# Kernel tuning notes

Hardware: AMD Instinct MI355X
Metric: run time of the kernel (lower is better)

The kernel has to match this reference:

```python
import jax, jax.numpy as jnp
import numpy as np

ITERATIONS = 20  # Resonator(iterations=20)
B, F, V, D = 128, 4, 2048, 4096


def _hardsign(x):
    # bipolar normalization used by MAP-VSA multiset(normalize=True); ties -> +1
    return jnp.where(x >= 0, 1.0, -1.0).astype(x.dtype)


def setup_inputs() -> dict:
    key = jax.random.key(0)
    k1, k2 = jax.random.split(key, 2)
    # bipolar codebooks: (F, V, D)
    codebooks = _hardsign(jax.random.normal(k1, (F, V, D), dtype=jnp.float32))
    # a realistic composite input: bind (elementwise product) of one codevector per factor
    idx = jax.random.randint(k2, (B, F), 0, V)                       # (B, F)
    chosen = codebooks[jnp.arange(F)[None, :], idx]                  # (B, F, D)
    inputs = jnp.prod(chosen, axis=1)                                # (B, D)
    # standard resonator init: normalized superposition of each codebook
    init_estimates = jnp.broadcast_to(
        _hardsign(jnp.sum(codebooks, axis=1)), (B, F, D)
    ).astype(jnp.float32)                                            # (B, F, D)
    return {"inputs": inputs, "init_estimates": init_estimates, "codebooks": codebooks}


def _resonator_step(inputs, est, codebooks):
    # est: (B, F, D). rolled stack over k=1..F-1 -> (B, F, F-1, D)
    f = est.shape[-2]
    rolled = jnp.stack([jnp.roll(est, k, axis=-2) for k in range(1, f)], axis=-2)
    inv_others = jnp.prod(rolled, axis=-2)          # multibind over dim -2 -> (B, F, D)
    new_est = inputs[:, None, :] * inv_others       # bind -> (B, F, D)
    sim = jnp.einsum('bfd,fvd->bfv', new_est, codebooks)   # similarity (activation='NONE')
    # multiset(codebooks, sim, normalize=True)
    return _hardsign(jnp.einsum('bfv,fvd->bfd', sim, codebooks))


def reference(inputs, init_estimates, codebooks):
    def body(carry, i):
        est, k, done = carry
        new = _resonator_step(inputs, est, codebooks)
        eq = jnp.all(new == est)          # convergence check (fixed point)
        k = jnp.where(done, k, i)
        return (new, k, done | eq), None

    carry0 = (init_estimates, jnp.int32(0), jnp.bool_(False))
    (est, k, _), _ = jax.lax.scan(body, carry0, jnp.arange(ITERATIONS, dtype=jnp.int32))
    # cleanup: argmax of |similarity| per factor (argmax_abs=True)
    sim = jnp.einsum('bfd,fvd->bfv', est, codebooks)
    outcome = jnp.argmax(jnp.abs(sim), axis=-1)     # (B, F) int indices
    return outcome, k
```

## Files before the change

### kernel.cpp

```cpp
#include <hip/hip_runtime.h>
#include <stdint.h>

#define B_    128
#define F_    4
#define V_    2048
#define D_    4096
#define DW    64
#define VW    32
#define ITERS 20
#define NKT   16
#define NBLK  512

typedef _Float16 half8 __attribute__((ext_vector_type(8)));
typedef float   floatx4 __attribute__((ext_vector_type(4)));

__device__ __forceinline__ uint64_t cload64(const uint64_t* p) {
    return __hip_atomic_load(p, __ATOMIC_RELAXED, __HIP_MEMORY_SCOPE_AGENT);
}
__device__ __forceinline__ void cstore64(uint64_t* p, uint64_t v) {
    __hip_atomic_store(p, v, __ATOMIC_RELAXED, __HIP_MEMORY_SCOPE_AGENT);
}
__device__ __forceinline__ ulonglong2 cload_u128(const uint64_t* p) {
    ulonglong2 r;
    r.x = cload64(p); r.y = cload64(p + 1);
    return r;
}
__device__ __forceinline__ half8 cload_h8(const _Float16* p) {
    union { uint64_t q[2]; half8 h; } u;
    u.q[0] = cload64((const uint64_t*)p);
    u.q[1] = cload64((const uint64_t*)p + 1);
    return u.h;
}

__device__ __forceinline__ void xbar(int* bar, int gen) {
    __syncthreads();
    if (threadIdx.x == 0) {
        int s = blockIdx.x & 15;
        int t = __hip_atomic_fetch_add(&bar[s * 16], 1, __ATOMIC_RELAXED,
                                       __HIP_MEMORY_SCOPE_AGENT);
        if (t == gen * (NBLK / 16) - 1)
            __hip_atomic_fetch_add(&bar[256], 1, __ATOMIC_RELAXED,
                                   __HIP_MEMORY_SCOPE_AGENT);
        int spins = 0;
        while (__hip_atomic_load(&bar[256], __ATOMIC_RELAXED,
                                 __HIP_MEMORY_SCOPE_AGENT) < gen * 16) {
            __builtin_amdgcn_s_sleep(2);
            if (++spins > (1 << 16)) break;
        }
    }
    __syncthreads();
}

__device__ __forceinline__ void pack16(const float* __restrict__ x,
                                       uint64_t* __restrict__ bits, int t) {
    const float4* p = (const float4*)x + (size_t)t * 4;
    uint32_t m = 0;
    #pragma unroll
    for (int j = 0; j < 4; ++j) {
        float4 v = p[j];
        m |= (__float_as_uint(v.x) >> 31) << (4 * j + 0);
        m |= (__float_as_uint(v.y) >> 31) << (4 * j + 1);
        m |= (__float_as_uint(v.z) >> 31) << (4 * j + 2);
        m |= (__float_as_uint(v.w) >> 31) << (4 * j + 3);
    }
    ((unsigned short*)bits)[t] = (unsigned short)m;
}

__global__ __launch_bounds__(256) void k_setup(
        const float* __restrict__ cb, const float* __restrict__ inite,
        const float* __restrict__ inputs,
        uint64_t* __restrict__ cb_bits, uint64_t* __restrict__ est_bits,
        uint64_t* __restrict__ in_bits,
        int* __restrict__ flags, int* __restrict__ keys) {
    int gtid = blockIdx.x * 256 + threadIdx.x;
    const int T = 512 * 256;
    const int ncb = (F_ * V_ * D_) / 16;
    for (int t = gtid; t < ncb; t += T) pack16(cb, cb_bits, t);
    pack16(inite, est_bits, gtid);
    if (gtid < (B_ * D_) / 16) pack16(inputs, in_bits, gtid);
    if (gtid < 32) flags[gtid] = 0;
    if (gtid < B_ * F_) keys[gtid] = 0;
}

__global__ void k_packT(const uint64_t* __restrict__ cb_bits,
                        uint64_t* __restrict__ cbT) {
    int vw = blockIdx.x, dwg = blockIdx.y, f = blockIdx.z;
    int lane = threadIdx.x & 63;
    int dw = dwg * 4 + (threadIdx.x >> 6);
    uint64_t w = cb_bits[((size_t)f * V_ + vw * 64 + lane) * DW + dw];
    uint64_t r = 0;
    for (int d2 = 0; d2 < 64; ++d2) {
        uint64_t m = __ballot((unsigned)((w >> d2) & 1));
        if (lane == d2) r = m;
    }
    cbT[((size_t)f * D_ + dw * 64 + lane) * VW + vw] = r;
}

__global__ __launch_bounds__(256, 2) void k_loop(
        const uint64_t* __restrict__ cb_bits, const uint64_t* __restrict__ cbT,
        uint64_t* __restrict__ est_bits, const uint64_t* __restrict__ in_bits,
        _Float16* __restrict__ simf, int* __restrict__ flags, int* bar) {
    const int bid = blockIdx.x;
    const int tid = threadIdx.x;
    int g = 0;

    __shared__ __align__(16) unsigned char LDSU[49152];
    __shared__ int bd;

    #pragma unroll 1
    for (int i = 0; i < ITERS; ++i) {
        {
            int vt = bid & 31, bt = (bid >> 5) & 3, f = bid >> 7;
            int v0 = vt * 64, b0 = bt * 32;
            ulonglong2* CB2 = (ulonglong2*)LDSU;
            ulonglong2* NB2 = (ulonglong2*)(LDSU + 32768);
            #pragma unroll
            for (int it = 0; it < 8; ++it) {
                int cq = it * 256 + tid;
                int r = cq >> 5, ch = cq & 31;
                const ulonglong2* src = (const ulonglong2*)(cb_bits + ((size_t)f * V_ + v0 + r) * DW);
                CB2[r * 32 + (ch ^ (r & 7))] = src[ch];
            }
            #pragma unroll
            for (int it = 0; it < 4; ++it) {
                int cq = it * 256 + tid;
                int r = cq >> 5, ch = cq & 31;
                int b = b0 + r;
                const ulonglong2* iv = (const ulonglong2*)(in_bits + (size_t)b * DW);
                const uint64_t* eb = est_bits + (size_t)b * F_ * DW;
                ulonglong2 i2 = iv[ch];
                ulonglong2 e0 = cload_u128(eb + 0 * DW + 2 * ch);
                ulonglong2 e1 = cload_u128(eb + 1 * DW + 2 * ch);
                ulonglong2 e2 = cload_u128(eb + 2 * DW + 2 * ch);
                ulonglong2 e3 = cload_u128(eb + 3 * DW + 2 * ch);
                uint64_t ex = (f == 0) ? e0.x : (f == 1) ? e1.x : (f == 2) ? e2.x : e3.x;
                uint64_t ey = (f == 0) ? e0.y : (f == 1) ? e1.y : (f == 2) ? e2.y : e3.y;
                ulonglong2 val;
                val.x = i2.x ^ e0.x ^ e1.x ^ e2.x ^ e3.x ^ ex;
                val.y = i2.y ^ e0.y ^ e1.y ^ e2.y ^ e3.y ^ ey;
                NB2[r * 32 + (ch ^ (r & 7))] = val;
            }
            __syncthreads();

            int vv = tid & 15, bb = tid >> 4;
            int svz = vv & 7, sbz = bb & 7;
            int pc[2][4];
            #pragma unroll
            for (int j = 0; j < 2; ++j)
                #pragma unroll
                for (int ii = 0; ii < 4; ++ii) pc[j][ii] = 0;

            #pragma unroll 4
            for (int ch = 0; ch < 32; ++ch) {
                ulonglong2 c[4], n[2];
                #pragma unroll
                for (int ii = 0; ii < 4; ++ii)
                    c[ii] = CB2[(vv + 16 * ii) * 32 + (ch ^ svz)];
                #pragma unroll
                for (int j = 0; j < 2; ++j)
                    n[j] = NB2[(bb + 16 * j) * 32 + (ch ^ sbz)];
                #pragma unroll
                for (int j = 0; j < 2; ++j)
                    #pragma unroll
                    for (int ii = 0; ii < 4; ++ii)
                        pc[j][ii] += __popcll(n[j].x ^ c[ii].x) + __popcll(n[j].y ^ c[ii].y);
            }
            #pragma unroll
            for (int j = 0; j < 2; ++j) {
                int b = b0 + bb + 16 * j;
                #pragma unroll
                for (int ii = 0; ii < 4; ++ii) {
                    int v = v0 + vv + 16 * ii;
                    union { _Float16 hf; unsigned short us; } cv;
                    cv.hf = (_Float16)(2048 - pc[j][ii]);
                    int other = __shfl_xor((int)cv.us, 1, 64);
                    if (!(vv & 1)) {
                        uint32_t packv = (uint32_t)cv.us | ((uint32_t)other << 16);
                        __hip_atomic_store(
                            (uint32_t*)&simf[((size_t)f * B_ + b) * V_ + v], packv,
                            __ATOMIC_RELAXED, __HIP_MEMORY_SCOPE_AGENT);
                    }
                }
            }
        }
        xbar(bar, ++g);

        {
            int gnt = bid & 63, gmt = (bid >> 6) & 1, gf = bid >> 7;
            int m0 = gmt * 64, n0 = gnt * 64;
            int lane = tid & 63, wave = tid >> 6;
            int lrow = lane & 15, lq = lane >> 4;
            int wm = wave & 1, wn = wave >> 1;

            uint64_t* Bb = (uint64_t*)LDSU;
            _Float16* As = (_Float16*)(LDSU + 16384);
            if (tid == 0) bd = 0;

            const uint64_t* bsrc = cbT + ((size_t)gf * D_ + n0) * VW;
            #pragma unroll
            for (int p = 0; p < 4; ++p) {
                int chunk = p * 256 + tid;
                int dloc = chunk >> 4, cw = chunk & 15;
                ulonglong2 val = *(const ulonglong2*)&bsrc[dloc * VW + cw * 2];
                *(ulonglong2*)&Bb[dloc * VW + ((cw ^ (dloc & 15)) * 2)] = val;
            }

            const _Float16* Ab = simf + (size_t)gf * B_ * V_ + (size_t)m0 * V_;
            int arow = tid >> 4, acol = tid & 15;
            half8 areg[4];
            #pragma unroll
            for (int p = 0; p < 4; ++p)
                areg[p] = cload_h8(&Ab[(size_t)(p * 16 + arow) * V_ + acol * 8]);

            floatx4 acc[2][2] = {};

            const uint64_t SPREAD = 0x1000200040008000ull;
            const uint64_t SMASK  = 0x8000800080008000ull;
            const uint64_t PONE   = 0x3C003C003C003C00ull;

            #pragma unroll 1
            for (int kt = 0; kt < NKT; ++kt) {
                __syncthreads();
                #pragma unroll
                for (int p = 0; p < 4; ++p)
                    *(half8*)&As[(p * 16 + arow) * 128 + ((acol ^ arow) * 8)] = areg[p];
                if (kt + 1 < NKT) {
                    #pragma unroll
                    for (int p = 0; p < 4; ++p)
                        areg[p] = cload_h8(&Ab[(size_t)(p * 16 + arow) * V_ + (kt + 1) * 128 + acol * 8]);
                }
                __syncthreads();

                ulonglong2 bw[2];
                #pragma unroll
                for (int nt2 = 0; nt2 < 2; ++nt2) {
                    int dloc = wn * 32 + nt2 * 16 + lrow;
                    bw[nt2] = *(const ulonglong2*)&Bb[dloc * VW + ((kt ^ (dloc & 15)) * 2)];
                }
                #pragma unroll
                for (int ks = 0; ks < 4; ++ks) {
                    half8 af[2];
                    #pragma unroll
                    for (int mt2 = 0; mt2 < 2; ++mt2) {
                        int row = wm * 32 + mt2 * 16 + lrow;
                        af[mt2] = *(const half8*)&As[row * 128 + (((ks * 4 + lq) ^ lrow) * 8)];
                    }
                    half8 bfrag[2];
                    #pragma unroll
                    for (int nt2 = 0; nt2 < 2; ++nt2) {
                        uint64_t w = (ks < 2) ? bw[nt2].x : bw[nt2].y;
                        uint32_t byte = (uint32_t)(w >> ((((ks & 1) * 4 + lq)) * 8)) & 0xFFu;
                        union { uint64_t q[2]; half8 h; } bu;
                        bu.q[0] = (((uint64_t)(byte & 0xFu) * SPREAD) & SMASK) ^ PONE;
                        bu.q[1] = (((uint64_t)(byte >> 4)   * SPREAD) & SMASK) ^ PONE;
                        bfrag[nt2] = bu.h;
                    }
                    #pragma unroll
                    for (int mt2 = 0; mt2 < 2; ++mt2)
                        #pragma unroll
                        for (int nt2 = 0; nt2 < 2; ++nt2)
                            acc[mt2][nt2] = __builtin_amdgcn_mfma_f32_16x16x32_f16(
                                af[mt2], bfrag[nt2], acc[mt2][nt2], 0, 0, 0);
                }
            }

            __syncthreads();
            unsigned char* S = (unsigned char*)As;
            #pragma unroll
            for (int mt2 = 0; mt2 < 2; ++mt2)
                #pragma unroll
                for (int nt2 = 0; nt2 < 2; ++nt2)
                    #pragma unroll
                    for (int r = 0; r < 4; ++r) {
                        int row = wm * 32 + mt2 * 16 + lq * 4 + r;
                        int col = wn * 32 + nt2 * 16 + lrow;
                        S[row * 64 + col] = (acc[mt2][nt2][r] < 0.0f) ? 1 : 0;
                    }
            __syncthreads();
            if (tid < 64) {
                const uint64_t* Sw = (const uint64_t*)S;
                uint64_t m = 0;
                #pragma unroll
                for (int j = 0; j < 8; ++j) {
                    uint64_t w = Sw[tid * 8 + j];
                    m |= ((w * 0x0102040810204080ull) >> 56) << (8 * j);
                }
                size_t widx = ((size_t)(m0 + tid) * F_ + gf) * DW + gnt;
                uint64_t old = cload64(&est_bits[widx]);
                cstore64(&est_bits[widx], m);
                if (old != m) atomicOr(&bd, 1);
            }
            __syncthreads();
            if (tid == 0 && bd) atomicOr(&flags[i], 1);
        }
        if (i + 1 < ITERS) xbar(bar, ++g);
    }
}

__global__ __launch_bounds__(256) void k_argmax(
        const uint64_t* __restrict__ cb_bits,
        const uint64_t* __restrict__ est_bits,
        int* __restrict__ keys) {
    int vt = blockIdx.x, f = blockIdx.y;
    int v0 = vt * 32;
    int tid = threadIdx.x;

    __shared__ __align__(16) ulonglong2 EB2[128 * 32];
    __shared__ __align__(16) ulonglong2 CBa[32 * 32];

    #pragma unroll
    for (int it = 0; it < 16; ++it) {
        int cq = it * 256 + tid;
        int r = cq >> 5, ch = cq & 31;
        const ulonglong2* src = (const ulonglong2*)(est_bits + ((size_t)r * F_ + f) * DW);
        EB2[r * 32 + (ch ^ (r & 7))] = src[ch];
    }
    #pragma unroll
    for (int it = 0; it < 4; ++it) {
        int cq = it * 256 + tid;
        int r = cq >> 5, ch = cq & 31;
        const ulonglong2* src = (const ulonglong2*)(cb_bits + ((size_t)f * V_ + v0 + r) * DW);
        CBa[r * 32 + (ch ^ (r & 7))] = src[ch];
    }
    __syncthreads();

    int vv = tid & 15, bb = tid >> 4;
    int svz = vv & 7, sbz = bb & 7;
    int pc[8][2];
    #pragma unroll
    for (int j = 0; j < 8; ++j) { pc[j][0] = 0; pc[j][1] = 0; }

    #pragma unroll 4
    for (int ch = 0; ch < 32; ++ch) {
        ulonglong2 c[2], n[8];
        #pragma unroll
        for (int i = 0; i < 2; ++i)
            c[i] = CBa[(vv + 16 * i) * 32 + (ch ^ svz)];
        #pragma unroll
        for (int j = 0; j < 8; ++j)
            n[j] = EB2[(bb + 16 * j) * 32 + (ch ^ sbz)];
        #pragma unroll
        for (int j = 0; j < 8; ++j)
            #pragma unroll
            for (int i = 0; i < 2; ++i)
                pc[j][i] += __popcll(n[j].x ^ c[i].x) + __popcll(n[j].y ^ c[i].y);
    }

    #pragma unroll
    for (int j = 0; j < 8; ++j) {
        int kj = (int)0x80000000;
        #pragma unroll
        for (int i = 0; i < 2; ++i) {
            int v = v0 + vv + 16 * i;
            int m = 2048 - pc[j][i]; if (m < 0) m = -m;
            int key = (m << 11) | (2047 - v);
            if (key > kj) kj = key;
        }
        #pragma unroll
        for (int s = 1; s < 16; s <<= 1) {
            int o = __shfl_xor(kj, s, 64);
            if (o > kj) kj = o;
        }
        if ((tid & 15) == 0)
            atomicMax(&keys[(size_t)(bb + 16 * j) * F_ + f], kj);
    }
}

__global__ void k_final(const int* __restrict__ keys, const int* __restrict__ flags,
                        int* __restrict__ out) {
    int tid = blockIdx.x * blockDim.x + threadIdx.x;
    if (tid < B_ * F_) out[tid] = 2047 - (keys[tid] & 0x7FF);
    if (tid == 0) {
        int k = ITERS - 1;
        for (int i = 0; i < ITERS; ++i) if (flags[i] == 0) { k = i; break; }
        out[B_ * F_] = k;
    }
}

extern "C" void kernel_launch(void* const* d_in, const int* in_sizes, int n_in,
                              void* d_out, int out_size, void* d_ws, size_t ws_size,
                              hipStream_t stream) {
    const float* inputs = (const float*)d_in[0];
    const float* inite  = (const float*)d_in[1];
    const float* cb     = (const float*)d_in[2];
    int* out = (int*)d_out;

    char* ws = (char*)d_ws;
    uint64_t* cb_bits  = (uint64_t*)ws;  ws += (size_t)F_ * V_ * DW * 8;
    uint64_t* cbT_bits = (uint64_t*)ws;  ws += (size_t)F_ * D_ * VW * 8;
    uint64_t* est_bits = (uint64_t*)ws;  ws += (size_t)B_ * F_ * DW * 8;
    uint64_t* in_bits  = (uint64_t*)ws;  ws += (size_t)B_ * DW * 8;
    _Float16* simf     = (_Float16*)ws;  ws += (size_t)F_ * B_ * V_ * 2;
    int*      flags    = (int*)ws;       ws += 32 * 4;
    int*      keys     = (int*)ws;       ws += B_ * F_ * 4;
    int*      bar      = (int*)ws;       ws += 2048;

    hipMemsetAsync(bar, 0, 2048, stream);

    k_setup<<<512, 256, 0, stream>>>(cb, inite, inputs, cb_bits, est_bits,
                                     in_bits, flags, keys);
    k_packT<<<dim3(32, 16, 4), 256, 0, stream>>>(cb_bits, cbT_bits);
    k_loop<<<NBLK, 256, 0, stream>>>(cb_bits, cbT_bits, est_bits, in_bits,
                                     simf, flags, bar);
    k_argmax<<<dim3(64, 4), 256, 0, stream>>>(cb_bits, est_bits, keys);
    k_final<<<2, 256, 0, stream>>>(keys, flags, out);
}
```

Measured before the change: 965.8 us.

## Use per-iteration buffers for estimates and similarities to allow plain cached loads

New measurement: 924.5 us. -4.3%, faster.

```diff
diff --git a/kernel.cpp b/kernel.cpp
--- a/kernel.cpp
+++ b/kernel.cpp
@@ -10,26 +10,17 @@
 #define ITERS 20
 #define NKT   16
 #define NBLK  512
+#define ESLOT (B_ * F_ * DW)
+#define SSLOT ((size_t)F_ * B_ * V_)
 
 typedef _Float16 half8 __attribute__((ext_vector_type(8)));
 typedef float   floatx4 __attribute__((ext_vector_type(4)));
 
-__device__ __forceinline__ uint64_t cload64(const uint64_t* p) {
-    return __hip_atomic_load(p, __ATOMIC_RELAXED, __HIP_MEMORY_SCOPE_AGENT);
-}
 __device__ __forceinline__ void cstore64(uint64_t* p, uint64_t v) {
     __hip_atomic_store(p, v, __ATOMIC_RELAXED, __HIP_MEMORY_SCOPE_AGENT);
 }
-__device__ __forceinline__ ulonglong2 cload_u128(const uint64_t* p) {
-    ulonglong2 r;
-    r.x = cload64(p); r.y = cload64(p + 1);
-    return r;
-}
-__device__ __forceinline__ half8 cload_h8(const _Float16* p) {
-    union { uint64_t q[2]; half8 h; } u;
-    u.q[0] = cload64((const uint64_t*)p);
-    u.q[1] = cload64((const uint64_t*)p + 1);
-    return u.h;
+__device__ __forceinline__ void cstore32(uint32_t* p, uint32_t v) {
+    __hip_atomic_store(p, v, __ATOMIC_RELAXED, __HIP_MEMORY_SCOPE_AGENT);
 }
 
 __device__ __forceinline__ void xbar(int* bar, int gen) {
@@ -69,14 +60,14 @@
 __global__ __launch_bounds__(256) void k_setup(
         const float* __restrict__ cb, const float* __restrict__ inite,
         const float* __restrict__ inputs,
-        uint64_t* __restrict__ cb_bits, uint64_t* __restrict__ est_bits,
+        uint64_t* __restrict__ cb_bits, uint64_t* __restrict__ est0,
         uint64_t* __restrict__ in_bits,
         int* __restrict__ flags, int* __restrict__ keys) {
     int gtid = blockIdx.x * 256 + threadIdx.x;
     const int T = 512 * 256;
     const int ncb = (F_ * V_ * D_) / 16;
     for (int t = gtid; t < ncb; t += T) pack16(cb, cb_bits, t);
-    pack16(inite, est_bits, gtid);
+    pack16(inite, est0, gtid);
     if (gtid < (B_ * D_) / 16) pack16(inputs, in_bits, gtid);
     if (gtid < 32) flags[gtid] = 0;
     if (gtid < B_ * F_) keys[gtid] = 0;
@@ -98,8 +89,8 @@
 
 __global__ __launch_bounds__(256, 2) void k_loop(
         const uint64_t* __restrict__ cb_bits, const uint64_t* __restrict__ cbT,
-        uint64_t* __restrict__ est_bits, const uint64_t* __restrict__ in_bits,
-        _Float16* __restrict__ simf, int* __restrict__ flags, int* bar) {
+        uint64_t* __restrict__ est_base, const uint64_t* __restrict__ in_bits,
+        _Float16* __restrict__ simf_base, int* __restrict__ flags, int* bar) {
     const int bid = blockIdx.x;
     const int tid = threadIdx.x;
     int g = 0;
@@ -109,6 +100,10 @@
 
     #pragma unroll 1
     for (int i = 0; i < ITERS; ++i) {
+        const uint64_t* esti = est_base + (size_t)i * ESLOT;
+        uint64_t*       esto = est_base + (size_t)(i + 1) * ESLOT;
+        _Float16*       simf = simf_base + (size_t)i * SSLOT;
+
         {
             int vt = bid & 31, bt = (bid >> 5) & 3, f = bid >> 7;
             int v0 = vt * 64, b0 = bt * 32;
@@ -127,12 +122,12 @@
                 int r = cq >> 5, ch = cq & 31;
                 int b = b0 + r;
                 const ulonglong2* iv = (const ulonglong2*)(in_bits + (size_t)b * DW);
-                const uint64_t* eb = est_bits + (size_t)b * F_ * DW;
+                const uint64_t* eb = esti + (size_t)b * F_ * DW;
                 ulonglong2 i2 = iv[ch];
-                ulonglong2 e0 = cload_u128(eb + 0 * DW + 2 * ch);
-                ulonglong2 e1 = cload_u128(eb + 1 * DW + 2 * ch);
-                ulonglong2 e2 = cload_u128(eb + 2 * DW + 2 * ch);
-                ulonglong2 e3 = cload_u128(eb + 3 * DW + 2 * ch);
+                ulonglong2 e0 = ((const ulonglong2*)(eb + 0 * DW))[ch];
+                ulonglong2 e1 = ((const ulonglong2*)(eb + 1 * DW))[ch];
+                ulonglong2 e2 = ((const ulonglong2*)(eb + 2 * DW))[ch];
+                ulonglong2 e3 = ((const ulonglong2*)(eb + 3 * DW))[ch];
                 uint64_t ex = (f == 0) ? e0.x : (f == 1) ? e1.x : (f == 2) ? e2.x : e3.x;
                 uint64_t ey = (f == 0) ? e0.y : (f == 1) ? e1.y : (f == 2) ? e2.y : e3.y;
                 ulonglong2 val;
@@ -176,9 +171,7 @@
                     int other = __shfl_xor((int)cv.us, 1, 64);
                     if (!(vv & 1)) {
                         uint32_t packv = (uint32_t)cv.us | ((uint32_t)other << 16);
-                        __hip_atomic_store(
-                            (uint32_t*)&simf[((size_t)f * B_ + b) * V_ + v], packv,
-                            __ATOMIC_RELAXED, __HIP_MEMORY_SCOPE_AGENT);
+                        cstore32((uint32_t*)&simf[((size_t)f * B_ + b) * V_ + v], packv);
                     }
                 }
             }
@@ -210,7 +203,7 @@
             half8 areg[4];
             #pragma unroll
             for (int p = 0; p < 4; ++p)
-                areg[p] = cload_h8(&Ab[(size_t)(p * 16 + arow) * V_ + acol * 8]);
+                areg[p] = *(const half8*)&Ab[(size_t)(p * 16 + arow) * V_ + acol * 8];
 
             floatx4 acc[2][2] = {};
 
@@ -227,7 +220,7 @@
                 if (kt + 1 < NKT) {
                     #pragma unroll
                     for (int p = 0; p < 4; ++p)
-                        areg[p] = cload_h8(&Ab[(size_t)(p * 16 + arow) * V_ + (kt + 1) * 128 + acol * 8]);
+                        areg[p] = *(const half8*)&Ab[(size_t)(p * 16 + arow) * V_ + (kt + 1) * 128 + acol * 8];
                 }
                 __syncthreads();
 
@@ -286,8 +279,8 @@
                     m |= ((w * 0x0102040810204080ull) >> 56) << (8 * j);
                 }
                 size_t widx = ((size_t)(m0 + tid) * F_ + gf) * DW + gnt;
-                uint64_t old = cload64(&est_bits[widx]);
-                cstore64(&est_bits[widx], m);
+                uint64_t old = esti[widx];
+                cstore64(&esto[widx], m);
                 if (old != m) atomicOr(&bd, 1);
             }
             __syncthreads();
@@ -388,20 +381,21 @@
     char* ws = (char*)d_ws;
     uint64_t* cb_bits  = (uint64_t*)ws;  ws += (size_t)F_ * V_ * DW * 8;
     uint64_t* cbT_bits = (uint64_t*)ws;  ws += (size_t)F_ * D_ * VW * 8;
-    uint64_t* est_bits = (uint64_t*)ws;  ws += (size_t)B_ * F_ * DW * 8;
+    uint64_t* est_base = (uint64_t*)ws;  ws += (size_t)(ITERS + 1) * ESLOT * 8;
     uint64_t* in_bits  = (uint64_t*)ws;  ws += (size_t)B_ * DW * 8;
-    _Float16* simf     = (_Float16*)ws;  ws += (size_t)F_ * B_ * V_ * 2;
+    _Float16* simf     = (_Float16*)ws;  ws += (size_t)ITERS * SSLOT * 2;
     int*      flags    = (int*)ws;       ws += 32 * 4;
     int*      keys     = (int*)ws;       ws += B_ * F_ * 4;
     int*      bar      = (int*)ws;       ws += 2048;
 
     hipMemsetAsync(bar, 0, 2048, stream);
 
-    k_setup<<<512, 256, 0, stream>>>(cb, inite, inputs, cb_bits, est_bits,
+    k_setup<<<512, 256, 0, stream>>>(cb, inite, inputs, cb_bits, est_base,
                                      in_bits, flags, keys);
     k_packT<<<dim3(32, 16, 4), 256, 0, stream>>>(cb_bits, cbT_bits);
-    k_loop<<<NBLK, 256, 0, stream>>>(cb_bits, cbT_bits, est_bits, in_bits,
+    k_loop<<<NBLK, 256, 0, stream>>>(cb_bits, cbT_bits, est_base, in_bits,
                                      simf, flags, bar);
-    k_argmax<<<dim3(64, 4), 256, 0, stream>>>(cb_bits, est_bits, keys);
+    k_argmax<<<dim3(64, 4), 256, 0, stream>>>(cb_bits,
+                                              est_base + (size_t)ITERS * ESLOT, keys);
     k_final<<<2, 256, 0, stream>>>(keys, flags, out);
 }
```
